# Performance work log

Measured on AMD Instinct MI355X. Metric: run time of the kernel, lower is better.

## Reference

```python
import jax, jax.numpy as jnp
import numpy as np

D_MODEL = 256
D_STATE = 64
D_CONV = 4
EXPAND = 2
HEADDIM = 64
D_INNER = EXPAND * D_MODEL            # 512
NHEADS = D_INNER // HEADDIM           # 8
D_XBC = D_INNER + 2 * D_STATE         # 640 (x, B, C; ngroups=1)
D_IN_PROJ = 2 * D_INNER + 2 * D_STATE + NHEADS  # 1160


def setup_inputs() -> dict:
    key = jax.random.key(0)
    ks = jax.random.split(key, 8)
    x = jax.random.normal(ks[0], (64, 5000, 12), jnp.float32)
    W_in = jax.random.normal(ks[1], (D_MODEL, D_IN_PROJ), jnp.float32) * 0.02
    conv_w = jax.random.normal(ks[2], (D_XBC, D_CONV), jnp.float32) * 0.1
    conv_b = jnp.zeros((D_XBC,), jnp.float32)
    A_log = jnp.log(jax.random.uniform(ks[3], (NHEADS,), jnp.float32, 1.0, 16.0))
    dt_bias = jax.random.normal(ks[4], (NHEADS,), jnp.float32) * 0.1
    D = jnp.ones((NHEADS,), jnp.float32)
    norm_w = jnp.ones((D_INNER,), jnp.float32)
    W_out = jax.random.normal(ks[5], (D_INNER, D_MODEL), jnp.float32) * 0.02
    return {"x": x, "W_in": W_in, "conv_w": conv_w, "conv_b": conv_b,
            "A_log": A_log, "dt_bias": dt_bias, "D": D,
            "norm_w": norm_w, "W_out": W_out}


def _mamba2(u, W_in, conv_w, conv_b, A_log, dt_bias, D, norm_w, W_out):
    b, l, _ = u.shape
    zxbcdt = u @ W_in                                   # (b,l,1160)
    z = zxbcdt[..., :D_INNER]                           # (b,l,512)
    xBC = zxbcdt[..., D_INNER:D_INNER + D_XBC]          # (b,l,640)
    dt = zxbcdt[..., D_INNER + D_XBC:]                  # (b,l,8)
    # causal depthwise conv1d (kernel 4) + SiLU
    xp = jnp.pad(xBC, ((0, 0), (D_CONV - 1, 0), (0, 0)))
    xBC = sum(xp[:, k:k + l, :] * conv_w[:, k] for k in range(D_CONV)) + conv_b
    xBC = jax.nn.silu(xBC)
    xs = xBC[..., :D_INNER].reshape(b, l, NHEADS, HEADDIM)
    Bm = xBC[..., D_INNER:D_INNER + D_STATE]            # (b,l,64)
    Cm = xBC[..., D_INNER + D_STATE:]                   # (b,l,64)
    dt = jax.nn.softplus(dt + dt_bias)                  # (b,l,h)
    A = -jnp.exp(A_log)                                 # (h,)

    def step(h, inp):
        x_t, dt_t, B_t, C_t = inp                       # (b,h,p),(b,h),(b,n),(b,n)
        decay = jnp.exp(dt_t * A)                       # (b,h)
        h = h * decay[..., None, None] + (dt_t[..., None] * x_t)[..., None] * B_t[:, None, None, :]
        y = jnp.einsum('bhpn,bn->bhp', h, C_t)
        return h, y

    h0 = jnp.zeros((b, NHEADS, HEADDIM, D_STATE), u.dtype)
    _, ys = jax.lax.scan(step, h0, (xs.transpose(1, 0, 2, 3), dt.transpose(1, 0, 2),
                                    Bm.transpose(1, 0, 2), Cm.transpose(1, 0, 2)))
    y = ys.transpose(1, 0, 2, 3) + D[None, None, :, None] * xs   # D skip, per head
    y = y.reshape(b, l, D_INNER)
    # RMSNormGated: gate then rmsnorm
    y = y * jax.nn.silu(z)
    y = y * jax.lax.rsqrt(jnp.mean(y * y, axis=-1, keepdims=True) + 1e-5) * norm_w
    return y @ W_out                                    # (b,l,256)


def reference(x, W_in, conv_w, conv_b, A_log, dt_bias, D, norm_w, W_out):
    b = x.shape[0]
    u = x.reshape(b, 250, 240)                          # 'b (t p1) f -> b t (p1 f)'
    u = jnp.pad(u, ((0, 0), (0, 0), (0, D_MODEL - 240)))
    y = _mamba2(u, W_in, conv_w, conv_b, A_log, dt_bias, D, norm_w, W_out)
    y = jax.nn.selu(y)                                  # AlphaDropout is identity at eval
    y = y[..., :240]
    return y.reshape(b, 5000, 12)
```

## Files before the change

kernel.cpp:

```cpp
#include <hip/hip_runtime.h>
#include <cstdint>
#include <cstddef>

#define D_MODEL 256
#define D_STATE 64
#define HEADDIM 64
#define D_INNER 512
#define NHEADS 8
#define D_XBC 640
#define NPROJ 1160
#define ZXW 1152
#define BATCH 64
#define SEQ 250
#define ROWS (BATCH * SEQ)
#define KIN 240
#define KPAD 256
#define NPAD 1216
#define TPAD 256

typedef __bf16 bf16x8 __attribute__((ext_vector_type(8)));
typedef float f32x4 __attribute__((ext_vector_type(4)));

__device__ __forceinline__ float readlane_f(float v, int lane) {
    return __uint_as_float(__builtin_amdgcn_readlane(__float_as_uint(v), lane));
}
__device__ __forceinline__ float silu_f(float x) { return x * (1.f / (1.f + __expf(-x))); }
__device__ __forceinline__ unsigned short bf16_rne(float f) {
    unsigned int u = __float_as_uint(f);
    u += 0x7fff + ((u >> 16) & 1);
    return (unsigned short)(u >> 16);
}
__device__ __forceinline__ float bf2f(unsigned short u) {
    return __uint_as_float(((unsigned int)u) << 16);
}
__device__ __forceinline__ unsigned int pack2(float a, float b) {
    return (unsigned int)bf16_rne(a) | ((unsigned int)bf16_rne(b) << 16);
}

#define NA (ROWS * KPAD)
#define NB (NPAD * KPAD)
#define NW (D_MODEL * D_INNER)
__global__ __launch_bounds__(256) void cast_all_kernel(const float* __restrict__ x,
                                                       const float* __restrict__ Win,
                                                       const float* __restrict__ Wout,
                                                       unsigned short* __restrict__ a_bf,
                                                       unsigned short* __restrict__ bt_bf,
                                                       unsigned short* __restrict__ wt_bf) {
    int idx = blockIdx.x * 256 + threadIdx.x;
    if (idx < NA) {
        int row = idx >> 8, c = idx & 255;
        float v = (c < KIN) ? x[row * KIN + c] : 0.f;
        a_bf[idx] = bf16_rne(v);
    } else if (idx < NA + NB) {
        int r = idx - NA;
        int n = r >> 8, k = r & 255;
        float v = (n < NPROJ && k < KIN) ? Win[k * NPROJ + n] : 0.f;
        bt_bf[r] = bf16_rne(v);
    } else if (idx < NA + NB + NW) {
        int r = idx - NA - NB;
        int n = r & 255, k = r >> 8;
        wt_bf[n * D_INNER + k] = bf16_rne(Wout[k * D_MODEL + n]);
    }
}

#define SA 40
__global__ __launch_bounds__(256) void gemm1_mfma(const unsigned short* __restrict__ A,
                                                  const unsigned short* __restrict__ Bt,
                                                  unsigned short* __restrict__ Czx,
                                                  float* __restrict__ dtraw) {
    __shared__ unsigned short As[128 * SA];
    __shared__ unsigned short Bs[64 * SA];
    const int tid = threadIdx.x;
    const int lane = tid & 63, wave = tid >> 6;
    const int wm = wave >> 1, wn = wave & 1;
    const int q = lane >> 4, l15 = lane & 15;
    const int rowBase = blockIdx.y * 128, colBase = blockIdx.x * 64;
    f32x4 acc[4][2] = {};

    const int sr = tid >> 2;
    const int sc = (tid & 3) * 8;

    for (int k0 = 0; k0 < KPAD; k0 += 32) {
        *(uint4*)&As[sr * SA + sc] =
            *(const uint4*)&A[(size_t)(rowBase + sr) * KPAD + k0 + sc];
        *(uint4*)&As[(sr + 64) * SA + sc] =
            *(const uint4*)&A[(size_t)(rowBase + sr + 64) * KPAD + k0 + sc];
        *(uint4*)&Bs[sr * SA + sc] =
            *(const uint4*)&Bt[(size_t)(colBase + sr) * KPAD + k0 + sc];
        __syncthreads();

        bf16x8 bfr[2];
#pragma unroll
        for (int nt = 0; nt < 2; nt++)
            bfr[nt] = *(const bf16x8*)&Bs[(wn * 32 + nt * 16 + l15) * SA + q * 8];
#pragma unroll
        for (int mt = 0; mt < 4; mt++) {
            bf16x8 afr = *(const bf16x8*)&As[(wm * 64 + mt * 16 + l15) * SA + q * 8];
#pragma unroll
            for (int nt = 0; nt < 2; nt++)
                acc[mt][nt] = __builtin_amdgcn_mfma_f32_16x16x32_bf16(afr, bfr[nt],
                                                                      acc[mt][nt], 0, 0, 0);
        }
        __syncthreads();
    }
#pragma unroll
    for (int mt = 0; mt < 4; mt++) {
        int grow0 = rowBase + wm * 64 + mt * 16 + q * 4;
#pragma unroll
        for (int nt = 0; nt < 2; nt++) {
            int gcol = colBase + wn * 32 + nt * 16 + l15;
            if (gcol < ZXW) {
#pragma unroll
                for (int reg = 0; reg < 4; reg++) {
                    unsigned int u = bf16_rne(acc[mt][nt][reg]);
                    unsigned int partner = (unsigned int)__shfl_xor((int)u, 1, 64);
                    if ((l15 & 1) == 0)
                        *(unsigned int*)&Czx[(size_t)(grow0 + reg) * ZXW + gcol] =
                            u | (partner << 16);
                }
            } else if (gcol < NPROJ) {
#pragma unroll
                for (int reg = 0; reg < 4; reg++)
                    dtraw[(size_t)(grow0 + reg) * NHEADS + (gcol - ZXW)] = acc[mt][nt][reg];
            }
        }
    }
}

#define CT_IN_STR 68
#define CT_TR_STR 70
__global__ __launch_bounds__(256) void conv_kernel(const unsigned short* __restrict__ zxbc,
                                                   const float* __restrict__ dtraw,
                                                   const float* __restrict__ conv_w,
                                                   const float* __restrict__ conv_b,
                                                   const float* __restrict__ dt_bias,
                                                   unsigned short* __restrict__ xc_bf,
                                                   unsigned short* __restrict__ xcT_bf,
                                                   float* __restrict__ dtp) {
    const int b = blockIdx.x;
    const int t0 = blockIdx.z * 64;
    if (blockIdx.y == 10) {
        for (int it = threadIdx.x; it < 512; it += 256) {
            int h = it & 7;
            int t = t0 + (it >> 3);
            if (t < SEQ) {
                float v = dtraw[(size_t)(b * SEQ + t) * NHEADS + h] + dt_bias[h];
                dtp[(size_t)(b * SEQ + t) * NHEADS + h] =
                    (v > 20.f) ? v : __logf(1.f + __expf(v));
            }
        }
        return;
    }
    __shared__ float In[67 * CT_IN_STR];
    __shared__ unsigned short OutT[64 * CT_TR_STR];
    const int cg = blockIdx.y;
    const int tid = threadIdx.x;
    const int lane = tid & 63;
    const int w = tid >> 6;
    const int ch = cg * 64 + lane;

    for (int r = w; r < 67; r += 4) {
        int t = t0 - 3 + r;
        float v = (t >= 0 && t < SEQ)
                      ? bf2f(zxbc[(size_t)(b * SEQ + t) * ZXW + D_INNER + ch])
                      : 0.f;
        In[r * CT_IN_STR + lane] = v;
    }
    __syncthreads();
    const float w0 = conv_w[ch * 4 + 0], w1 = conv_w[ch * 4 + 1];
    const float w2 = conv_w[ch * 4 + 2], w3 = conv_w[ch * 4 + 3];
    const float bias = conv_b[ch];
    unsigned short vals[16];
#pragma unroll
    for (int i = 0; i < 16; i++) {
        int tt = w * 16 + i;
        float acc = fmaf(w3, In[(tt + 3) * CT_IN_STR + lane],
                    fmaf(w2, In[(tt + 2) * CT_IN_STR + lane],
                    fmaf(w1, In[(tt + 1) * CT_IN_STR + lane],
                    fmaf(w0, In[tt * CT_IN_STR + lane], bias))));
        float sv = silu_f(acc);
        unsigned short bv = (t0 + tt < SEQ) ? bf16_rne(sv) : (unsigned short)0;
        vals[i] = bv;
        OutT[lane * CT_TR_STR + tt] = bv;
    }
#pragma unroll
    for (int i = 0; i < 16; i++) {
        int tt = w * 16 + i;
        if (t0 + tt < SEQ)
            xc_bf[(size_t)(b * SEQ + t0 + tt) * D_XBC + ch] = vals[i];
    }
    __syncthreads();
    unsigned short* dstbase = xcT_bf + ((size_t)b * D_XBC + cg * 64) * TPAD + t0;
#pragma unroll
    for (int i = 0; i < 16; i++) {
        int c2 = w * 16 + i;
        dstbase[(size_t)c2 * TPAD + lane] = OutT[c2 * CT_TR_STR + lane];
    }
}

#define LSTR 72
__global__ __launch_bounds__(256) void scan_intra(const unsigned short* __restrict__ xc_bf,
                                                  const unsigned short* __restrict__ xcT_bf,
                                                  const float* __restrict__ dtp,
                                                  const float* __restrict__ A_log,
                                                  const float* __restrict__ Dvec,
                                                  unsigned short* __restrict__ yout_bf,
                                                  unsigned short* __restrict__ st_g) {
    __shared__ unsigned short C_l[64 * LSTR];
    __shared__ unsigned short BP_l[64 * LSTR];
    __shared__ unsigned short XT_l[64 * LSTR];
    __shared__ float cs_s[64], dts_s[64], fws_s[64];

    const int blk = blockIdx.x;
    const int bh = blk >> 2, c = blk & 3;
    const int b = bh >> 3, h = bh & 7;
    const int tid = threadIdx.x;
    const int lane = tid & 63, w = tid >> 6;
    const int q = lane >> 4, l15 = lane & 15;
    const int t0 = c * 64;
    const float A = -__expf(A_log[h]);
    const float Dh = Dvec[h];

    const int r = tid >> 2, c0 = (tid & 3) * 16;

    {
        if (t0 + r < SEQ) {
            const unsigned short* rowp = xc_bf + (size_t)(b * SEQ + t0 + r) * D_XBC;
            *(uint4*)&C_l[r * LSTR + c0] = *(const uint4*)&rowp[D_INNER + D_STATE + c0];
            *(uint4*)&C_l[r * LSTR + c0 + 8] =
                *(const uint4*)&rowp[D_INNER + D_STATE + c0 + 8];
            *(uint4*)&BP_l[r * LSTR + c0] = *(const uint4*)&rowp[D_INNER + c0];
            *(uint4*)&BP_l[r * LSTR + c0 + 8] = *(const uint4*)&rowp[D_INNER + c0 + 8];
        } else {
            uint4 z = {0, 0, 0, 0};
            *(uint4*)&C_l[r * LSTR + c0] = z;
            *(uint4*)&C_l[r * LSTR + c0 + 8] = z;
            *(uint4*)&BP_l[r * LSTR + c0] = z;
            *(uint4*)&BP_l[r * LSTR + c0 + 8] = z;
        }
        const unsigned short* xrow =
            xcT_bf + ((size_t)b * D_XBC + h * HEADDIM + r) * TPAD + t0;
        *(uint4*)&XT_l[r * LSTR + c0] = *(const uint4*)&xrow[c0];
        *(uint4*)&XT_l[r * LSTR + c0 + 8] = *(const uint4*)&xrow[c0 + 8];
    }
    uint4 braw0, braw1;
    {
        const unsigned short* brow =
            xcT_bf + ((size_t)b * D_XBC + D_INNER + r) * TPAD + t0 + c0;
        braw0 = *(const uint4*)&brow[0];
        braw1 = *(const uint4*)&brow[8];
    }
    if (w == 0) {
        int t = lane;
        float dtv = (t0 + t < SEQ) ? dtp[(size_t)(b * SEQ + t0 + t) * NHEADS + h] : 0.f;
        float csv = dtv * A;
#pragma unroll
        for (int o = 1; o < 64; o <<= 1) {
            float u = __shfl_up(csv, o, 64);
            if (lane >= o) csv += u;
        }
        float tot = readlane_f(csv, 63);
        cs_s[t] = csv;
        dts_s[t] = dtv;
        fws_s[t] = dtv * __expf(tot - csv);
    }
    __syncthreads();

    f32x4 g[4] = {};
#pragma unroll
    for (int k0 = 0; k0 < 64; k0 += 32) {
        bf16x8 ca = *(const bf16x8*)&C_l[(w * 16 + l15) * LSTR + k0 + q * 8];
#pragma unroll
        for (int nt = 0; nt < 4; nt++) {
            bf16x8 bb = *(const bf16x8*)&BP_l[(nt * 16 + l15) * LSTR + k0 + q * 8];
            g[nt] = __builtin_amdgcn_mfma_f32_16x16x32_bf16(ca, bb, g[nt], 0, 0, 0);
        }
    }
    __syncthreads();

    {
        unsigned short tmp[16];
        const unsigned short* rp = (const unsigned short*)&braw0;
#pragma unroll
        for (int j = 0; j < 8; j++) tmp[j] = bf16_rne(bf2f(rp[j]) * fws_s[c0 + j]);
        rp = (const unsigned short*)&braw1;
#pragma unroll
        for (int j = 0; j < 8; j++) tmp[8 + j] = bf16_rne(bf2f(rp[j]) * fws_s[c0 + 8 + j]);
        *(uint4*)&C_l[r * LSTR + c0] = *(uint4*)&tmp[0];
        *(uint4*)&C_l[r * LSTR + c0 + 8] = *(uint4*)&tmp[8];
    }
#pragma unroll
    for (int nt = 0; nt < 4; nt++) {
#pragma unroll
        for (int rr = 0; rr < 4; rr++) {
            int t = w * 16 + q * 4 + rr;
            int s = nt * 16 + l15;
            float pv = 0.f;
            if (s <= t) {
                pv = g[nt][rr] * __expf(cs_s[t] - cs_s[s]) * dts_s[s];
                if (s == t) pv += Dh;
            }
            unsigned int u = bf16_rne(pv);
            unsigned int partner = (unsigned int)__shfl_xor((int)u, 1, 64);
            if ((l15 & 1) == 0)
                *(unsigned int*)&BP_l[t * LSTR + nt * 16 + l15] = u | (partner << 16);
        }
    }
    __syncthreads();

    f32x4 y[4] = {};
#pragma unroll
    for (int k0 = 0; k0 < 64; k0 += 32) {
        bf16x8 pa = *(const bf16x8*)&BP_l[(w * 16 + l15) * LSTR + k0 + q * 8];
#pragma unroll
        for (int nt = 0; nt < 4; nt++) {
            bf16x8 xb = *(const bf16x8*)&XT_l[(nt * 16 + l15) * LSTR + k0 + q * 8];
            y[nt] = __builtin_amdgcn_mfma_f32_16x16x32_bf16(pa, xb, y[nt], 0, 0, 0);
        }
    }
    if (c < 3) {
        f32x4 st[4] = {};
#pragma unroll
        for (int k0 = 0; k0 < 64; k0 += 32) {
            bf16x8 xa = *(const bf16x8*)&XT_l[(w * 16 + l15) * LSTR + k0 + q * 8];
#pragma unroll
            for (int nt = 0; nt < 4; nt++) {
                bf16x8 bwb = *(const bf16x8*)&C_l[(nt * 16 + l15) * LSTR + k0 + q * 8];
                st[nt] = __builtin_amdgcn_mfma_f32_16x16x32_bf16(xa, bwb, st[nt], 0, 0, 0);
            }
        }
        unsigned short* stc = st_g + ((size_t)(bh * 3 + c)) * 4096;
#pragma unroll
        for (int nt = 0; nt < 4; nt++)
#pragma unroll
            for (int rr = 0; rr < 4; rr++) {
                unsigned int u = bf16_rne(st[nt][rr]);
                unsigned int partner = (unsigned int)__shfl_xor((int)u, 1, 64);
                if ((l15 & 1) == 0)
                    *(unsigned int*)&stc[(w * 16 + q * 4 + rr) * 64 + nt * 16 + l15] =
                        u | (partner << 16);
            }
    }
#pragma unroll
    for (int nt = 0; nt < 4; nt++)
#pragma unroll
        for (int rr = 0; rr < 4; rr++) {
            int t = w * 16 + q * 4 + rr;
            if (t0 + t < SEQ) {
                int p = nt * 16 + l15;
                unsigned int u = bf16_rne(y[nt][rr]);
                unsigned int partner = (unsigned int)__shfl_xor((int)u, 1, 64);
                if ((l15 & 1) == 0)
                    *(unsigned int*)&yout_bf[(size_t)(b * SEQ + t0 + t) * D_INNER +
                                             h * HEADDIM + p] = u | (partner << 16);
            }
        }
}

__global__ __launch_bounds__(256) void scan_inter(const unsigned short* __restrict__ xc_bf,
                                                  const float* __restrict__ dtp,
                                                  const float* __restrict__ A_log,
                                                  unsigned short* __restrict__ yout_bf,
                                                  const unsigned short* __restrict__ st_g) {
    __shared__ unsigned short C_l[64 * LSTR];
    __shared__ unsigned short h_l[64 * LSTR];
    __shared__ float cs_s[64];
    __shared__ float csum[4];

    const int blk = blockIdx.x;
    const int bh = blk / 3, c = (blk - bh * 3) + 1;
    const int b = bh >> 3, h = bh & 7;
    const int tid = threadIdx.x;
    const int lane = tid & 63, w = tid >> 6;
    const int q = lane >> 4, l15 = lane & 15;
    const int t0 = c * 64;
    const float A = -__expf(A_log[h]);

    {
        int t = lane;
        int gt = w * 64 + t;
        float dtv = (gt < SEQ) ? dtp[(size_t)(b * SEQ + gt) * NHEADS + h] : 0.f;
        float csv = dtv * A;
#pragma unroll
        for (int o = 1; o < 64; o <<= 1) {
            float u = __shfl_up(csv, o, 64);
            if (lane >= o) csv += u;
        }
        if (w == c) cs_s[t] = csv;
        if (lane == 63) csum[w] = csv;
    }
    {
        int r = tid >> 2, c0 = (tid & 3) * 16;
        if (t0 + r < SEQ) {
            const unsigned short* rowp = xc_bf + (size_t)(b * SEQ + t0 + r) * D_XBC;
            *(uint4*)&C_l[r * LSTR + c0] = *(const uint4*)&rowp[D_INNER + D_STATE + c0];
            *(uint4*)&C_l[r * LSTR + c0 + 8] =
                *(const uint4*)&rowp[D_INNER + D_STATE + c0 + 8];
        } else {
            uint4 z = {0, 0, 0, 0};
            *(uint4*)&C_l[r * LSTR + c0] = z;
            *(uint4*)&C_l[r * LSTR + c0 + 8] = z;
        }
    }
    __syncthreads();

    {
        float wgt[3];
        for (int cp = 0; cp < c; cp++) {
            float s = 0.f;
            for (int j = cp + 1; j < c; j++) s += csum[j];
            wgt[cp] = __expf(s);
        }
        const unsigned short* stb = st_g + (size_t)bh * 3 * 4096;
        for (int i = tid; i < 4096; i += 256) {
            float acc = 0.f;
            for (int cp = 0; cp < c; cp++) acc += wgt[cp] * bf2f(stb[cp * 4096 + i]);
            h_l[(i >> 6) * LSTR + (i & 63)] = bf16_rne(acc);
        }
    }
    __syncthreads();

    f32x4 in[4] = {};
#pragma unroll
    for (int k0 = 0; k0 < 64; k0 += 32) {
        bf16x8 ca = *(const bf16x8*)&C_l[(w * 16 + l15) * LSTR + k0 + q * 8];
#pragma unroll
        for (int nt = 0; nt < 4; nt++) {
            bf16x8 hb = *(const bf16x8*)&h_l[(nt * 16 + l15) * LSTR + k0 + q * 8];
            in[nt] = __builtin_amdgcn_mfma_f32_16x16x32_bf16(ca, hb, in[nt], 0, 0, 0);
        }
    }
#pragma unroll
    for (int nt = 0; nt < 4; nt++)
#pragma unroll
        for (int r = 0; r < 4; r++) {
            int t = w * 16 + q * 4 + r;
            if (t0 + t < SEQ) {
                int p = nt * 16 + l15;
                size_t ai = (size_t)(b * SEQ + t0 + t) * D_INNER + h * HEADDIM + p;
                float alpha = __expf(cs_s[t]);
                float nv = bf2f(yout_bf[ai]) + alpha * in[nt][r];
                unsigned int u = bf16_rne(nv);
                unsigned int partner = (unsigned int)__shfl_xor((int)u, 1, 64);
                if ((l15 & 1) == 0)
                    *(unsigned int*)&yout_bf[ai] = u | (partner << 16);
            }
        }
}

__global__ __launch_bounds__(256) void gate_kernel(const unsigned short* __restrict__ yout_bf,
                                                   const unsigned short* __restrict__ zxbc,
                                                   const float* __restrict__ norm_w,
                                                   unsigned short* __restrict__ g_bf) {
    const int wid = threadIdx.x >> 6, lane = threadIdx.x & 63;
    const int row = blockIdx.x * 4 + wid;
    const unsigned short* yr = yout_bf + (size_t)row * D_INNER;
    const unsigned short* zr = zxbc + (size_t)row * ZXW;
    const int c0 = lane * 8;
    uint4 yp = *(const uint4*)&yr[c0];
    uint4 zp = *(const uint4*)&zr[c0];
    const unsigned short* ys = (const unsigned short*)&yp;
    const unsigned short* zs = (const unsigned short*)&zp;
    float g[8];
#pragma unroll
    for (int i = 0; i < 8; i++) g[i] = bf2f(ys[i]) * silu_f(bf2f(zs[i]));
    float s = 0.f;
#pragma unroll
    for (int i = 0; i < 8; i++) s = fmaf(g[i], g[i], s);
#pragma unroll
    for (int o = 32; o; o >>= 1) s += __shfl_xor(s, o, 64);
    float rms = rsqrtf(s * (1.f / 512.f) + 1e-5f);
    float4 w0 = *(const float4*)&norm_w[c0], w1 = *(const float4*)&norm_w[c0 + 4];
    uint4 pk;
    pk.x = pack2(g[0] * rms * w0.x, g[1] * rms * w0.y);
    pk.y = pack2(g[2] * rms * w0.z, g[3] * rms * w0.w);
    pk.z = pack2(g[4] * rms * w1.x, g[5] * rms * w1.y);
    pk.w = pack2(g[6] * rms * w1.z, g[7] * rms * w1.w);
    *(uint4*)&g_bf[(size_t)row * D_INNER + c0] = pk;
}

__global__ __launch_bounds__(256) void gemm2_mfma(const unsigned short* __restrict__ A,
                                                  const unsigned short* __restrict__ Bt,
                                                  float* __restrict__ out) {
    __shared__ unsigned short As[128 * SA];
    __shared__ unsigned short Bs[64 * SA];
    const int tid = threadIdx.x;
    const int lane = tid & 63, wave = tid >> 6;
    const int wm = wave >> 1, wn = wave & 1;
    const int q = lane >> 4, l15 = lane & 15;
    const int rowBase = blockIdx.y * 128, colBase = blockIdx.x * 64;
    f32x4 acc[4][2] = {};

    const int sr = tid >> 2;
    const int sc = (tid & 3) * 8;

    for (int k0 = 0; k0 < D_INNER; k0 += 32) {
        *(float4*)&As[sr * SA + sc] =
            *(const float4*)&A[(size_t)(rowBase + sr) * D_INNER + k0 + sc];
        *(float4*)&As[(sr + 64) * SA + sc] =
            *(const float4*)&A[(size_t)(rowBase + sr + 64) * D_INNER + k0 + sc];
        *(float4*)&Bs[sr * SA + sc] =
            *(const float4*)&Bt[(size_t)(colBase + sr) * D_INNER + k0 + sc];
        __syncthreads();

        bf16x8 bfr[2];
#pragma unroll
        for (int nt = 0; nt < 2; nt++)
            bfr[nt] = *(const bf16x8*)&Bs[(wn * 32 + nt * 16 + l15) * SA + q * 8];
#pragma unroll
        for (int mt = 0; mt < 4; mt++) {
            bf16x8 afr = *(const bf16x8*)&As[(wm * 64 + mt * 16 + l15) * SA + q * 8];
#pragma unroll
            for (int nt = 0; nt < 2; nt++)
                acc[mt][nt] = __builtin_amdgcn_mfma_f32_16x16x32_bf16(afr, bfr[nt],
                                                                      acc[mt][nt], 0, 0, 0);
        }
        __syncthreads();
    }
    const float SC = 1.0507009873554805f, AL = 1.6732632423543772f;
#pragma unroll
    for (int mt = 0; mt < 4; mt++) {
        int grow = rowBase + wm * 64 + mt * 16 + q * 4;
#pragma unroll
        for (int nt = 0; nt < 2; nt++) {
            int gcol = colBase + wn * 32 + nt * 16 + l15;
            if (gcol < 240) {
#pragma unroll
                for (int reg = 0; reg < 4; reg++) {
                    float v = acc[mt][nt][reg];
                    v = (v > 0.f) ? SC * v : SC * AL * (__expf(v) - 1.f);
                    out[(size_t)(grow + reg) * 240 + gcol] = v;
                }
            }
        }
    }
}

extern "C" void kernel_launch(void* const* d_in, const int* in_sizes, int n_in,
                              void* d_out, int out_size, void* d_ws, size_t ws_size,
                              hipStream_t stream) {
    const float* x = (const float*)d_in[0];
    const float* W_in = (const float*)d_in[1];
    const float* conv_w = (const float*)d_in[2];
    const float* conv_b = (const float*)d_in[3];
    const float* A_log = (const float*)d_in[4];
    const float* dt_bias = (const float*)d_in[5];
    const float* Dv = (const float*)d_in[6];
    const float* norm_w = (const float*)d_in[7];
    const float* W_out = (const float*)d_in[8];
    float* out = (float*)d_out;

    unsigned short* us = (unsigned short*)d_ws;
    unsigned short* zxbc_bf = us;
    unsigned short* xc_bf = zxbc_bf + (size_t)ROWS * ZXW;
    unsigned short* xcT_bf = xc_bf + (size_t)ROWS * D_XBC;
    unsigned short* yout_bf = xcT_bf + (size_t)BATCH * D_XBC * TPAD;
    unsigned short* st_g = yout_bf + (size_t)ROWS * D_INNER;
    unsigned short* bt_bf = st_g + (size_t)512 * 3 * 4096;
    unsigned short* wt_bf = bt_bf + (size_t)NPAD * KPAD;
    unsigned short* g_bf = wt_bf + (size_t)D_MODEL * D_INNER;
    float* dtraw = (float*)(g_bf + (size_t)ROWS * D_INNER);
    float* dtp = dtraw + (size_t)ROWS * NHEADS;
    unsigned short* a_bf = (unsigned short*)(dtp + (size_t)ROWS * NHEADS);

    int cast_total = NA + NB + NW;
    cast_all_kernel<<<dim3((cast_total + 255) / 256), 256, 0, stream>>>(x, W_in, W_out,
                                                                        a_bf, bt_bf, wt_bf);

    gemm1_mfma<<<dim3(NPAD / 64, ROWS / 128), 256, 0, stream>>>(a_bf, bt_bf, zxbc_bf, dtraw);

    conv_kernel<<<dim3(BATCH, 11, 4), 256, 0, stream>>>(zxbc_bf, dtraw, conv_w, conv_b,
                                                        dt_bias, xc_bf, xcT_bf, dtp);

    scan_intra<<<dim3(BATCH * NHEADS * 4), 256, 0, stream>>>(xc_bf, xcT_bf, dtp, A_log, Dv,
                                                             yout_bf, st_g);

    scan_inter<<<dim3(BATCH * NHEADS * 3), 256, 0, stream>>>(xc_bf, dtp, A_log,
                                                             yout_bf, st_g);

    gate_kernel<<<dim3(ROWS / 4), 256, 0, stream>>>(yout_bf, zxbc_bf, norm_w, g_bf);

    gemm2_mfma<<<dim3(D_MODEL / 64, ROWS / 128), 256, 0, stream>>>(g_bf, wt_bf, out);
}
```

Measured before the change: 213.6 us.

## Fuse gated RMSNorm into output projection GEMM with per-row rescale

Removes the separate gate kernel and its bf16 intermediate buffer. The output GEMM now computes y*silu(z)*norm_w on the fly while loading A tiles, accumulates the sum of squares per row, and applies the rms scale to the accumulator before SELU. Tiling changes to 32 rows by all 256 output columns per block, giving 500 blocks. Each block reloads the full W_out slice every k-step, and the normalised values are rounded to bf16 before rms scaling, which slightly changes the numerics.

```diff
diff --git a/kernel.cpp b/kernel.cpp
--- a/kernel.cpp
+++ b/kernel.cpp
@@ -448,88 +448,86 @@
         }
 }
 
-__global__ __launch_bounds__(256) void gate_kernel(const unsigned short* __restrict__ yout_bf,
+__global__ __launch_bounds__(256) void gemm2_fused(const unsigned short* __restrict__ yout_bf,
                                                    const unsigned short* __restrict__ zxbc,
+                                                   const unsigned short* __restrict__ Bt,
                                                    const float* __restrict__ norm_w,
-                                                   unsigned short* __restrict__ g_bf) {
-    const int wid = threadIdx.x >> 6, lane = threadIdx.x & 63;
-    const int row = blockIdx.x * 4 + wid;
-    const unsigned short* yr = yout_bf + (size_t)row * D_INNER;
-    const unsigned short* zr = zxbc + (size_t)row * ZXW;
-    const int c0 = lane * 8;
-    uint4 yp = *(const uint4*)&yr[c0];
-    uint4 zp = *(const uint4*)&zr[c0];
-    const unsigned short* ys = (const unsigned short*)&yp;
-    const unsigned short* zs = (const unsigned short*)&zp;
-    float g[8];
-#pragma unroll
-    for (int i = 0; i < 8; i++) g[i] = bf2f(ys[i]) * silu_f(bf2f(zs[i]));
-    float s = 0.f;
-#pragma unroll
-    for (int i = 0; i < 8; i++) s = fmaf(g[i], g[i], s);
-#pragma unroll
-    for (int o = 32; o; o >>= 1) s += __shfl_xor(s, o, 64);
-    float rms = rsqrtf(s * (1.f / 512.f) + 1e-5f);
-    float4 w0 = *(const float4*)&norm_w[c0], w1 = *(const float4*)&norm_w[c0 + 4];
-    uint4 pk;
-    pk.x = pack2(g[0] * rms * w0.x, g[1] * rms * w0.y);
-    pk.y = pack2(g[2] * rms * w0.z, g[3] * rms * w0.w);
-    pk.z = pack2(g[4] * rms * w1.x, g[5] * rms * w1.y);
-    pk.w = pack2(g[6] * rms * w1.z, g[7] * rms * w1.w);
-    *(uint4*)&g_bf[(size_t)row * D_INNER + c0] = pk;
-}
-
-__global__ __launch_bounds__(256) void gemm2_mfma(const unsigned short* __restrict__ A,
-                                                  const unsigned short* __restrict__ Bt,
-                                                  float* __restrict__ out) {
-    __shared__ unsigned short As[128 * SA];
-    __shared__ unsigned short Bs[64 * SA];
+                                                   float* __restrict__ out) {
+    __shared__ unsigned short As[32 * SA];
+    __shared__ unsigned short Bs[256 * SA];
+    __shared__ float rms_s[32];
     const int tid = threadIdx.x;
-    const int lane = tid & 63, wave = tid >> 6;
-    const int wm = wave >> 1, wn = wave & 1;
+    const int lane = tid & 63;
+    const int wn = tid >> 6;
     const int q = lane >> 4, l15 = lane & 15;
-    const int rowBase = blockIdx.y * 128, colBase = blockIdx.x * 64;
-    f32x4 acc[4][2] = {};
-
-    const int sr = tid >> 2;
-    const int sc = (tid & 3) * 8;
+    const int rowBase = blockIdx.x * 32;
+    f32x4 acc[2][4] = {};
+
+    const int tr = tid >> 3;
+    const int tk = (tid & 7) * 4;
+
+    const unsigned short* yrow = yout_bf + (size_t)(rowBase + tr) * D_INNER + tk;
+    const unsigned short* zrow = zxbc + (size_t)(rowBase + tr) * ZXW + tk;
+    float ssq = 0.f;
 
     for (int k0 = 0; k0 < D_INNER; k0 += 32) {
-        *(float4*)&As[sr * SA + sc] =
-            *(const float4*)&A[(size_t)(rowBase + sr) * D_INNER + k0 + sc];
-        *(float4*)&As[(sr + 64) * SA + sc] =
-            *(const float4*)&A[(size_t)(rowBase + sr + 64) * D_INNER + k0 + sc];
-        *(float4*)&Bs[sr * SA + sc] =
-            *(const float4*)&Bt[(size_t)(colBase + sr) * D_INNER + k0 + sc];
+        uint2 yp = *(const uint2*)&yrow[k0];
+        uint2 zp = *(const uint2*)&zrow[k0];
+        float4 nw = *(const float4*)&norm_w[k0 + tk];
+        const unsigned short* ys = (const unsigned short*)&yp;
+        const unsigned short* zs = (const unsigned short*)&zp;
+        float g0 = bf2f(ys[0]) * silu_f(bf2f(zs[0]));
+        float g1 = bf2f(ys[1]) * silu_f(bf2f(zs[1]));
+        float g2 = bf2f(ys[2]) * silu_f(bf2f(zs[2]));
+        float g3 = bf2f(ys[3]) * silu_f(bf2f(zs[3]));
+        ssq = fmaf(g0, g0, ssq);
+        ssq = fmaf(g1, g1, ssq);
+        ssq = fmaf(g2, g2, ssq);
+        ssq = fmaf(g3, g3, ssq);
+        uint2 pk;
+        pk.x = pack2(g0 * nw.x, g1 * nw.y);
+        pk.y = pack2(g2 * nw.z, g3 * nw.w);
+        *(uint2*)&As[tr * SA + tk] = pk;
+        const unsigned short* brow = Bt + (size_t)tid * D_INNER + k0;
+        *(uint4*)&Bs[tid * SA + 0] = *(const uint4*)&brow[0];
+        *(uint4*)&Bs[tid * SA + 8] = *(const uint4*)&brow[8];
+        *(uint4*)&Bs[tid * SA + 16] = *(const uint4*)&brow[16];
+        *(uint4*)&Bs[tid * SA + 24] = *(const uint4*)&brow[24];
         __syncthreads();
 
-        bf16x8 bfr[2];
-#pragma unroll
-        for (int nt = 0; nt < 2; nt++)
-            bfr[nt] = *(const bf16x8*)&Bs[(wn * 32 + nt * 16 + l15) * SA + q * 8];
-#pragma unroll
-        for (int mt = 0; mt < 4; mt++) {
-            bf16x8 afr = *(const bf16x8*)&As[(wm * 64 + mt * 16 + l15) * SA + q * 8];
-#pragma unroll
-            for (int nt = 0; nt < 2; nt++)
+        bf16x8 bfr[4];
+#pragma unroll
+        for (int nt = 0; nt < 4; nt++)
+            bfr[nt] = *(const bf16x8*)&Bs[(wn * 64 + nt * 16 + l15) * SA + q * 8];
+#pragma unroll
+        for (int mt = 0; mt < 2; mt++) {
+            bf16x8 afr = *(const bf16x8*)&As[(mt * 16 + l15) * SA + q * 8];
+#pragma unroll
+            for (int nt = 0; nt < 4; nt++)
                 acc[mt][nt] = __builtin_amdgcn_mfma_f32_16x16x32_bf16(afr, bfr[nt],
                                                                       acc[mt][nt], 0, 0, 0);
         }
         __syncthreads();
     }
+    ssq += __shfl_xor(ssq, 1, 64);
+    ssq += __shfl_xor(ssq, 2, 64);
+    ssq += __shfl_xor(ssq, 4, 64);
+    if ((tid & 7) == 0) rms_s[tr] = rsqrtf(ssq * (1.f / 512.f) + 1e-5f);
+    __syncthreads();
+
     const float SC = 1.0507009873554805f, AL = 1.6732632423543772f;
 #pragma unroll
-    for (int mt = 0; mt < 4; mt++) {
-        int grow = rowBase + wm * 64 + mt * 16 + q * 4;
-#pragma unroll
-        for (int nt = 0; nt < 2; nt++) {
-            int gcol = colBase + wn * 32 + nt * 16 + l15;
+    for (int mt = 0; mt < 2; mt++) {
+        int lrow0 = mt * 16 + q * 4;
+#pragma unroll
+        for (int nt = 0; nt < 4; nt++) {
+            int gcol = wn * 64 + nt * 16 + l15;
             if (gcol < 240) {
 #pragma unroll
                 for (int reg = 0; reg < 4; reg++) {
-                    float v = acc[mt][nt][reg];
+                    float v = acc[mt][nt][reg] * rms_s[lrow0 + reg];
                     v = (v > 0.f) ? SC * v : SC * AL * (__expf(v) - 1.f);
-                    out[(size_t)(grow + reg) * 240 + gcol] = v;
+                    out[(size_t)(rowBase + lrow0 + reg) * 240 + gcol] = v;
                 }
             }
         }
@@ -558,8 +556,7 @@
     unsigned short* st_g = yout_bf + (size_t)ROWS * D_INNER;
     unsigned short* bt_bf = st_g + (size_t)512 * 3 * 4096;
     unsigned short* wt_bf = bt_bf + (size_t)NPAD * KPAD;
-    unsigned short* g_bf = wt_bf + (size_t)D_MODEL * D_INNER;
-    float* dtraw = (float*)(g_bf + (size_t)ROWS * D_INNER);
+    float* dtraw = (float*)(wt_bf + (size_t)D_MODEL * D_INNER);
     float* dtp = dtraw + (size_t)ROWS * NHEADS;
     unsigned short* a_bf = (unsigned short*)(dtp + (size_t)ROWS * NHEADS);
 
@@ -578,7 +575,5 @@
     scan_inter<<<dim3(BATCH * NHEADS * 3), 256, 0, stream>>>(xc_bf, dtp, A_log,
                                                              yout_bf, st_g);
 
-    gate_kernel<<<dim3(ROWS / 4), 256, 0, stream>>>(yout_bf, zxbc_bf, norm_w, g_bf);
-
-    gemm2_mfma<<<dim3(D_MODEL / 64, ROWS / 128), 256, 0, stream>>>(g_bf, wt_bf, out);
-}
+    gemm2_fused<<<dim3(ROWS / 32), 256, 0, stream>>>(yout_bf, zxbc_bf, wt_bf, norm_w, out);
+}
```

New measurement: 209.9 us. No clear change (-1.7%).
